# Kernel optimization log

Hardware: AMD Instinct MI355X
Metric: run time of the kernel (lower is better)

## Reference

```python
import jax, jax.numpy as jnp
import numpy as np

B, H, SQ, SKV, D = 4, 16, 2048, 2048, 128
SCALE = float(np.sqrt(D))  # scale_factor passed to forward; q_k is divided by it


def setup_inputs() -> dict:
    key = jax.random.key(0)
    kq, kk, kv = jax.random.split(key, 3)
    q = jax.random.normal(kq, (B, H, SQ, D), dtype=jnp.float32)
    k = jax.random.normal(kk, (B, H, SKV, D), dtype=jnp.float32)
    v = jax.random.normal(kv, (B, H, SKV, D), dtype=jnp.float32)
    return {"q": q, "k": k, "v": v}


def reference(q, k, v):
    # q_k = q @ k^T, divided by scale_factor
    scores = jnp.einsum("bhqd,bhkd->bhqk", q, k) / SCALE  # [B,H,Sq,Skv]
    attn = jax.nn.softmax(scores, axis=-1)
    # dropout(p=0.1) is identity in eval/inference mode
    out = jnp.einsum("bhqk,bhkd->bhqd", attn, v)  # [B,H,Sq,D]
    return out
```

## Files before the change

### kernel.cpp

```cpp
#include <hip/hip_runtime.h>
#include <hip/hip_bf16.h>

#define B_ 4
#define H_ 16
#define SQ 2048
#define SKV 2048
#define D_ 128
#define BH (B_*H_)
#define BM 128
#define BN 32
#define NITER (SKV/BN)

typedef __attribute__((ext_vector_type(8))) short bf16x8;
typedef __attribute__((ext_vector_type(4))) float f32x4;

__device__ inline unsigned short f2bf(float f) {
    union { float f; unsigned u; } x{f};
    unsigned r = x.u + 0x7fffu + ((x.u >> 16) & 1u);
    return (unsigned short)(r >> 16);
}

#if defined(__has_builtin) && __has_builtin(__builtin_amdgcn_cvt_pk_bf16_f32)
#define PKBF16(a,b) ({ auto _r = __builtin_amdgcn_cvt_pk_bf16_f32((a),(b)); \
                       unsigned _u; __builtin_memcpy(&_u, &_r, 4); _u; })
#else
#define PKBF16(a,b) ((unsigned)f2bf(a) | ((unsigned)f2bf(b) << 16))
#endif

__device__ inline void gl_lds16(const short* g, short* l) {
    __builtin_amdgcn_global_load_lds((const __attribute__((address_space(1))) unsigned*)g,
                                     (__attribute__((address_space(3))) unsigned*)l,
                                     16, 0, 0);
}

__global__ __launch_bounds__(256) void prep(const float* __restrict__ kin,
                                            const float* __restrict__ vin,
                                            short* __restrict__ kbf,
                                            short* __restrict__ vtg) {
    __shared__ short tile[64 * 136];
    int bx = blockIdx.x, tid = threadIdx.x;
    if (bx < 8192) {
        const float4* s = (const float4*)kin;
        uint2* d = (uint2*)kbf;
        int i = bx * 256 + tid;
        const int HALF = (BH * SKV * D_ / 4) / 2;
#pragma unroll
        for (int h = 0; h < 2; ++h) {
            int j = i + h * HALF;
            float4 a = s[j];
            d[j] = make_uint2(PKBF16(a.x, a.y), PKBF16(a.z, a.w));
        }
    } else {
        int bx2 = bx - 8192;
        int bh = bx2 >> 5;
        int t0 = (bx2 & 31) * 64;
        {
            int r = tid >> 4, cg = tid & 15;
#pragma unroll
            for (int s = 0; s < 4; ++s) {
                int rr = r + s * 16;
                const float* p = vin + ((size_t)bh * SKV + t0 + rr) * D_ + cg * 8;
                float4 a = *(const float4*)p;
                float4 b = *(const float4*)(p + 4);
                union { unsigned u[4]; bf16x8 v; } f;
                f.u[0] = PKBF16(a.x, a.y); f.u[1] = PKBF16(a.z, a.w);
                f.u[2] = PKBF16(b.x, b.y); f.u[3] = PKBF16(b.z, b.w);
                *(bf16x8*)&tile[rr * 136 + cg * 8] = f.v;
            }
        }
        __syncthreads();
        {
            int row = tid >> 3;
            int c8 = tid & 7;
#pragma unroll
            for (int s = 0; s < 4; ++s) {
                int d = row + s * 32;
                union { short u[8]; uint4 q; } o;
#pragma unroll
                for (int j = 0; j < 8; ++j) o.u[j] = tile[(c8 * 8 + j) * 136 + d];
                *(uint4*)(vtg + ((size_t)bh * D_ + d) * SKV + t0 + c8 * 8) = o.q;
            }
        }
    }
}

__global__ __launch_bounds__(256, 3) void fa_kernel(const float* __restrict__ q,
                                                    const short* __restrict__ kbf,
                                                    const short* __restrict__ vtg,
                                                    float* __restrict__ out) {
    __shared__ short Ksh[2 * 32 * 128];
    __shared__ short Vsh[2 * 128 * 32];
    __shared__ short Psh[4 * 32 * 40];

    const int tid = threadIdx.x;
    const int wave = tid >> 6;
    const int lane = tid & 63;
    const int l16 = lane & 15;
    const int quad = lane >> 4;

    const int bx = blockIdx.x;
    const int qt = bx & 15;
    const int bh = bx >> 4;
    const int qrow0 = qt * BM + wave * 32;

    const float cscale = 1.4426950408889634f * 0.08838834764831845f;

    bf16x8 qf[2][4];
#pragma unroll
    for (int mt = 0; mt < 2; ++mt) {
        int row = qrow0 + mt * 16 + l16;
        const float* qp = q + ((size_t)bh * SQ + row) * D_ + quad * 8;
#pragma unroll
        for (int ks = 0; ks < 4; ++ks) {
            const float* p = qp + ks * 32;
            float4 a = *(const float4*)p;
            float4 b = *(const float4*)(p + 4);
            union { unsigned u[4]; bf16x8 v; } f;
            f.u[0] = PKBF16(a.x * cscale, a.y * cscale);
            f.u[1] = PKBF16(a.z * cscale, a.w * cscale);
            f.u[2] = PKBF16(b.x * cscale, b.y * cscale);
            f.u[3] = PKBF16(b.z * cscale, b.w * cscale);
            qf[mt][ks] = f.v;
        }
    }

    f32x4 oacc[8][2];
#pragma unroll
    for (int dt = 0; dt < 8; ++dt)
#pragma unroll
        for (int mt = 0; mt < 2; ++mt) oacc[dt][mt] = (f32x4)0.f;
    float lsum[2] = {0.f, 0.f};

    const short* kbase = kbf + (size_t)bh * SKV * D_;
    const short* vbase = vtg + (size_t)bh * D_ * SKV;
    const int krow0 = wave * 4 + (lane >> 4);
    const int kc8 = (lane & 15) ^ krow0;
    const short* kg = kbase + krow0 * 128 + kc8 * 8;
    short* const klbase = Ksh + wave * 512;
    const int vd0 = wave * 16 + (lane >> 2);
    const int vc = (lane & 3) ^ ((lane >> 2) & 3);
    const short* vg = vbase + (size_t)vd0 * SKV + vc * 8;
    short* const vlbase = Vsh + wave * 512;

    short* const pwav = Psh + wave * 1280;

    auto stage = [&](int it, int bufo) {
        const short* kgi = kg + it * (BN * D_);
        const short* vgi = vg + it * BN;
#pragma unroll
        for (int s = 0; s < 2; ++s) {
            gl_lds16(kgi + s * 2048, klbase + bufo + s * 2048);
            gl_lds16(vgi + (size_t)s * 64 * SKV, vlbase + bufo + s * 2048);
        }
    };

    auto compute = [&](int bufo) {
        f32x4 sacc[2][2];
#pragma unroll
        for (int kt = 0; kt < 2; ++kt) { sacc[kt][0] = (f32x4)0.f; sacc[kt][1] = (f32x4)0.f; }
#pragma unroll
        for (int kt = 0; kt < 2; ++kt)
#pragma unroll
            for (int ks = 0; ks < 4; ++ks) {
                bf16x8 kf = *(const bf16x8*)&Ksh[bufo + (kt * 16 + l16) * 128 + (((ks * 4 + quad) ^ l16) << 3)];
                sacc[kt][0] = __builtin_amdgcn_mfma_f32_16x16x32_bf16(kf, qf[0][ks], sacc[kt][0], 0, 0, 0);
                sacc[kt][1] = __builtin_amdgcn_mfma_f32_16x16x32_bf16(kf, qf[1][ks], sacc[kt][1], 0, 0, 0);
            }
#pragma unroll
        for (int mt = 0; mt < 2; ++mt) {
            short* pw = pwav + (mt * 16 + l16) * 40;
#pragma unroll
            for (int kt = 0; kt < 2; ++kt) {
                float p0 = __builtin_amdgcn_exp2f(sacc[kt][mt][0]);
                float p1 = __builtin_amdgcn_exp2f(sacc[kt][mt][1]);
                float p2 = __builtin_amdgcn_exp2f(sacc[kt][mt][2]);
                float p3 = __builtin_amdgcn_exp2f(sacc[kt][mt][3]);
                lsum[mt] += (p0 + p1) + (p2 + p3);
                *(uint2*)(pw + kt * 16 + quad * 4) = make_uint2(PKBF16(p0, p1), PKBF16(p2, p3));
            }
        }
        bf16x8 pa0 = *(const bf16x8*)(pwav + l16 * 40 + quad * 8);
        bf16x8 pa1 = *(const bf16x8*)(pwav + (16 + l16) * 40 + quad * 8);
#pragma unroll
        for (int dt = 0; dt < 8; ++dt) {
            bf16x8 vf = *(const bf16x8*)&Vsh[bufo + (dt * 16 + l16) * 32 + ((quad ^ (l16 & 3)) << 3)];
            oacc[dt][0] = __builtin_amdgcn_mfma_f32_16x16x32_bf16(vf, pa0, oacc[dt][0], 0, 0, 0);
            oacc[dt][1] = __builtin_amdgcn_mfma_f32_16x16x32_bf16(vf, pa1, oacc[dt][1], 0, 0, 0);
        }
    };

    stage(0, 0);
    for (int it = 0; it < NITER; it += 2) {
        __syncthreads();
        stage(it + 1, 4096);
        compute(0);
        __syncthreads();
        if (it + 2 < NITER) stage(it + 2, 0);
        compute(4096);
    }

#pragma unroll
    for (int mt = 0; mt < 2; ++mt) {
        lsum[mt] += __shfl_xor(lsum[mt], 16);
        lsum[mt] += __shfl_xor(lsum[mt], 32);
    }
    const float rl[2] = {1.0f / lsum[0], 1.0f / lsum[1]};
#pragma unroll
    for (int mt = 0; mt < 2; ++mt) {
        float* op = out + ((size_t)bh * SQ + qrow0 + mt * 16 + l16) * D_ + quad * 4;
#pragma unroll
        for (int dt = 0; dt < 8; ++dt) {
            f32x4 v = oacc[dt][mt] * rl[mt];
            *(f32x4*)(op + dt * 16) = v;
        }
    }
}

extern "C" void kernel_launch(void* const* d_in, const int* in_sizes, int n_in,
                              void* d_out, int out_size, void* d_ws, size_t ws_size,
                              hipStream_t stream) {
    const float* q = (const float*)d_in[0];
    const float* k = (const float*)d_in[1];
    const float* v = (const float*)d_in[2];
    float* out = (float*)d_out;

    short* kbf = (short*)d_ws;
    short* vtg = kbf + (size_t)BH * SKV * D_;

    prep<<<8192 + 2048, 256, 0, stream>>>(k, v, kbf, vtg);
    fa_kernel<<<BH * (SQ / BM), 256, 0, stream>>>(q, kbf, vtg, out);
}
```

Baseline: 380.6 us.

## Double query rows per wave for more K/V reuse and rewrite V transpose

Raises the query tile per block from 128 to 256 rows, so each wave handles 64 rows (four 16-row MFMA tiles) instead of 32. Each K/V tile staged into LDS is then reused by twice as many query rows, which halves the global K/V traffic and the staging/barrier overhead per unit of work. The cost is higher register pressure (larger Q and accumulator sets), hence launch bounds drop to 2 blocks per SM, and the grid has half as many blocks. The prep kernel's V transpose is also rewritten to pack bf16 pairs into a padded 32-bit LDS tile with vectorized reads, and the V LDS swizzle pattern is changed to match.

```diff
diff --git a/kernel.cpp b/kernel.cpp
--- a/kernel.cpp
+++ b/kernel.cpp
@@ -7,7 +7,7 @@
 #define SKV 2048
 #define D_ 128
 #define BH (B_*H_)
-#define BM 128
+#define BM 256
 #define BN 32
 #define NITER (SKV/BN)
 
@@ -37,7 +37,7 @@
                                             const float* __restrict__ vin,
                                             short* __restrict__ kbf,
                                             short* __restrict__ vtg) {
-    __shared__ short tile[64 * 136];
+    __shared__ unsigned tile[128 * 33];
     int bx = blockIdx.x, tid = threadIdx.x;
     if (bx < 8192) {
         const float4* s = (const float4*)kin;
@@ -54,43 +54,42 @@
         int bx2 = bx - 8192;
         int bh = bx2 >> 5;
         int t0 = (bx2 & 31) * 64;
-        {
-            int r = tid >> 4, cg = tid & 15;
-#pragma unroll
-            for (int s = 0; s < 4; ++s) {
-                int rr = r + s * 16;
-                const float* p = vin + ((size_t)bh * SKV + t0 + rr) * D_ + cg * 8;
-                float4 a = *(const float4*)p;
-                float4 b = *(const float4*)(p + 4);
-                union { unsigned u[4]; bf16x8 v; } f;
-                f.u[0] = PKBF16(a.x, a.y); f.u[1] = PKBF16(a.z, a.w);
-                f.u[2] = PKBF16(b.x, b.y); f.u[3] = PKBF16(b.z, b.w);
-                *(bf16x8*)&tile[rr * 136 + cg * 8] = f.v;
-            }
+        int kvp = tid >> 4, dc = tid & 15;
+#pragma unroll
+        for (int s = 0; s < 2; ++s) {
+            int pi = kvp + s * 16;
+            const float* r0 = vin + ((size_t)bh * SKV + t0 + 2 * pi) * D_ + dc * 8;
+            const float* r1 = r0 + D_;
+            float4 a0 = *(const float4*)r0, b0 = *(const float4*)(r0 + 4);
+            float4 a1 = *(const float4*)r1, b1 = *(const float4*)(r1 + 4);
+            unsigned* tb = &tile[(dc * 8) * 33 + pi];
+            tb[0 * 33] = PKBF16(a0.x, a1.x);
+            tb[1 * 33] = PKBF16(a0.y, a1.y);
+            tb[2 * 33] = PKBF16(a0.z, a1.z);
+            tb[3 * 33] = PKBF16(a0.w, a1.w);
+            tb[4 * 33] = PKBF16(b0.x, b1.x);
+            tb[5 * 33] = PKBF16(b0.y, b1.y);
+            tb[6 * 33] = PKBF16(b0.z, b1.z);
+            tb[7 * 33] = PKBF16(b0.w, b1.w);
         }
         __syncthreads();
-        {
-            int row = tid >> 3;
-            int c8 = tid & 7;
-#pragma unroll
-            for (int s = 0; s < 4; ++s) {
-                int d = row + s * 32;
-                union { short u[8]; uint4 q; } o;
-#pragma unroll
-                for (int j = 0; j < 8; ++j) o.u[j] = tile[(c8 * 8 + j) * 136 + d];
-                *(uint4*)(vtg + ((size_t)bh * D_ + d) * SKV + t0 + c8 * 8) = o.q;
-            }
-        }
-    }
-}
-
-__global__ __launch_bounds__(256, 3) void fa_kernel(const float* __restrict__ q,
+        int drow = tid >> 3, kvc = tid & 7;
+#pragma unroll
+        for (int ss = 0; ss < 4; ++ss) {
+            int d = drow + ss * 32;
+            uint4 w = *(const uint4*)&tile[d * 33 + kvc * 4];
+            *(uint4*)(vtg + ((size_t)bh * D_ + d) * SKV + t0 + kvc * 8) = w;
+        }
+    }
+}
+
+__global__ __launch_bounds__(256, 2) void fa_kernel(const float* __restrict__ q,
                                                     const short* __restrict__ kbf,
                                                     const short* __restrict__ vtg,
                                                     float* __restrict__ out) {
     __shared__ short Ksh[2 * 32 * 128];
     __shared__ short Vsh[2 * 128 * 32];
-    __shared__ short Psh[4 * 32 * 40];
+    __shared__ short Psh[4 * 64 * 40];
 
     const int tid = threadIdx.x;
     const int wave = tid >> 6;
@@ -99,15 +98,15 @@
     const int quad = lane >> 4;
 
     const int bx = blockIdx.x;
-    const int qt = bx & 15;
-    const int bh = bx >> 4;
-    const int qrow0 = qt * BM + wave * 32;
+    const int qt = bx & 7;
+    const int bh = bx >> 3;
+    const int qrow0 = qt * BM + wave * 64;
 
     const float cscale = 1.4426950408889634f * 0.08838834764831845f;
 
-    bf16x8 qf[2][4];
-#pragma unroll
-    for (int mt = 0; mt < 2; ++mt) {
+    bf16x8 qf[4][4];
+#pragma unroll
+    for (int mt = 0; mt < 4; ++mt) {
         int row = qrow0 + mt * 16 + l16;
         const float* qp = q + ((size_t)bh * SQ + row) * D_ + quad * 8;
 #pragma unroll
@@ -124,68 +123,69 @@
         }
     }
 
-    f32x4 oacc[8][2];
+    f32x4 oacc[8][4];
 #pragma unroll
     for (int dt = 0; dt < 8; ++dt)
 #pragma unroll
-        for (int mt = 0; mt < 2; ++mt) oacc[dt][mt] = (f32x4)0.f;
-    float lsum[2] = {0.f, 0.f};
+        for (int mt = 0; mt < 4; ++mt) oacc[dt][mt] = (f32x4)0.f;
+    float lsum[4] = {0.f, 0.f, 0.f, 0.f};
 
     const short* kbase = kbf + (size_t)bh * SKV * D_;
     const short* vbase = vtg + (size_t)bh * D_ * SKV;
-    const int krow0 = wave * 4 + (lane >> 4);
-    const int kc8 = (lane & 15) ^ krow0;
-    const short* kg = kbase + krow0 * 128 + kc8 * 8;
-    short* const klbase = Ksh + wave * 512;
-    const int vd0 = wave * 16 + (lane >> 2);
-    const int vc = (lane & 3) ^ ((lane >> 2) & 3);
-    const short* vg = vbase + (size_t)vd0 * SKV + vc * 8;
-    short* const vlbase = Vsh + wave * 512;
-
-    short* const pwav = Psh + wave * 1280;
+    const int kr = wave * 4 + (lane >> 4);
+    const int kc = (lane & 15) ^ kr;
+    const short* kg = kbase + kr * 128 + kc * 8;
+    const int vrow = wave * 16 + (lane >> 2);
+    const int vc = (lane & 3) ^ ((lane >> 3) & 3);
+    const short* vg = vbase + (size_t)vrow * SKV + vc * 8;
+    short* const klb = Ksh + wave * 512;
+    short* const vlb = Vsh + wave * 512;
+    short* const pwav = Psh + wave * 2560;
 
     auto stage = [&](int it, int bufo) {
         const short* kgi = kg + it * (BN * D_);
         const short* vgi = vg + it * BN;
 #pragma unroll
         for (int s = 0; s < 2; ++s) {
-            gl_lds16(kgi + s * 2048, klbase + bufo + s * 2048);
-            gl_lds16(vgi + (size_t)s * 64 * SKV, vlbase + bufo + s * 2048);
+            gl_lds16(kgi + s * 2048, klb + bufo + s * 2048);
+            gl_lds16(vgi + (size_t)s * 64 * SKV, vlb + bufo + s * 2048);
         }
     };
 
     auto compute = [&](int bufo) {
-        f32x4 sacc[2][2];
-#pragma unroll
-        for (int kt = 0; kt < 2; ++kt) { sacc[kt][0] = (f32x4)0.f; sacc[kt][1] = (f32x4)0.f; }
-#pragma unroll
-        for (int kt = 0; kt < 2; ++kt)
+#pragma unroll
+        for (int kt = 0; kt < 2; ++kt) {
+            f32x4 sacc[4];
+#pragma unroll
+            for (int mt = 0; mt < 4; ++mt) sacc[mt] = (f32x4)0.f;
 #pragma unroll
             for (int ks = 0; ks < 4; ++ks) {
                 bf16x8 kf = *(const bf16x8*)&Ksh[bufo + (kt * 16 + l16) * 128 + (((ks * 4 + quad) ^ l16) << 3)];
-                sacc[kt][0] = __builtin_amdgcn_mfma_f32_16x16x32_bf16(kf, qf[0][ks], sacc[kt][0], 0, 0, 0);
-                sacc[kt][1] = __builtin_amdgcn_mfma_f32_16x16x32_bf16(kf, qf[1][ks], sacc[kt][1], 0, 0, 0);
+#pragma unroll
+                for (int mt = 0; mt < 4; ++mt)
+                    sacc[mt] = __builtin_amdgcn_mfma_f32_16x16x32_bf16(kf, qf[mt][ks], sacc[mt], 0, 0, 0);
             }
 #pragma unroll
-        for (int mt = 0; mt < 2; ++mt) {
-            short* pw = pwav + (mt * 16 + l16) * 40;
-#pragma unroll
-            for (int kt = 0; kt < 2; ++kt) {
-                float p0 = __builtin_amdgcn_exp2f(sacc[kt][mt][0]);
-                float p1 = __builtin_amdgcn_exp2f(sacc[kt][mt][1]);
-                float p2 = __builtin_amdgcn_exp2f(sacc[kt][mt][2]);
-                float p3 = __builtin_amdgcn_exp2f(sacc[kt][mt][3]);
+            for (int mt = 0; mt < 4; ++mt) {
+                float p0 = __builtin_amdgcn_exp2f(sacc[mt][0]);
+                float p1 = __builtin_amdgcn_exp2f(sacc[mt][1]);
+                float p2 = __builtin_amdgcn_exp2f(sacc[mt][2]);
+                float p3 = __builtin_amdgcn_exp2f(sacc[mt][3]);
                 lsum[mt] += (p0 + p1) + (p2 + p3);
-                *(uint2*)(pw + kt * 16 + quad * 4) = make_uint2(PKBF16(p0, p1), PKBF16(p2, p3));
+                *(uint2*)&pwav[(mt * 16 + l16) * 40 + kt * 16 + quad * 4] =
+                    make_uint2(PKBF16(p0, p1), PKBF16(p2, p3));
             }
         }
-        bf16x8 pa0 = *(const bf16x8*)(pwav + l16 * 40 + quad * 8);
-        bf16x8 pa1 = *(const bf16x8*)(pwav + (16 + l16) * 40 + quad * 8);
+        bf16x8 pa[4];
+#pragma unroll
+        for (int mt = 0; mt < 4; ++mt)
+            pa[mt] = *(const bf16x8*)&pwav[(mt * 16 + l16) * 40 + quad * 8];
 #pragma unroll
         for (int dt = 0; dt < 8; ++dt) {
-            bf16x8 vf = *(const bf16x8*)&Vsh[bufo + (dt * 16 + l16) * 32 + ((quad ^ (l16 & 3)) << 3)];
-            oacc[dt][0] = __builtin_amdgcn_mfma_f32_16x16x32_bf16(vf, pa0, oacc[dt][0], 0, 0, 0);
-            oacc[dt][1] = __builtin_amdgcn_mfma_f32_16x16x32_bf16(vf, pa1, oacc[dt][1], 0, 0, 0);
+            bf16x8 vf = *(const bf16x8*)&Vsh[bufo + (dt * 16 + l16) * 32 + ((quad ^ ((l16 >> 1) & 3)) << 3)];
+#pragma unroll
+            for (int mt = 0; mt < 4; ++mt)
+                oacc[dt][mt] = __builtin_amdgcn_mfma_f32_16x16x32_bf16(vf, pa[mt], oacc[dt][mt], 0, 0, 0);
         }
     };
 
@@ -200,17 +200,17 @@
     }
 
 #pragma unroll
-    for (int mt = 0; mt < 2; ++mt) {
+    for (int mt = 0; mt < 4; ++mt) {
         lsum[mt] += __shfl_xor(lsum[mt], 16);
         lsum[mt] += __shfl_xor(lsum[mt], 32);
     }
-    const float rl[2] = {1.0f / lsum[0], 1.0f / lsum[1]};
-#pragma unroll
-    for (int mt = 0; mt < 2; ++mt) {
+#pragma unroll
+    for (int mt = 0; mt < 4; ++mt) {
+        float rl = 1.0f / lsum[mt];
         float* op = out + ((size_t)bh * SQ + qrow0 + mt * 16 + l16) * D_ + quad * 4;
 #pragma unroll
         for (int dt = 0; dt < 8; ++dt) {
-            f32x4 v = oacc[dt][mt] * rl[mt];
+            f32x4 v = oacc[dt][mt] * rl;
             *(f32x4*)(op + dt * 16) = v;
         }
     }
```

New measurement: 622.2 us. 63.5% more time.
